# Kernel optimization log

Measured on AMD Instinct MI355X. Metric: run time of the kernel, lower is better.

Reference implementation:

```python
import jax, jax.numpy as jnp
import numpy as np

B, L, H = 32, 512, 1024
H2 = H // 2          # split half = 512
D_ATTN = 64
EPS = 1e-5


def setup_inputs() -> dict:
    key = jax.random.key(0)
    ks = jax.random.split(key, 6)
    x = jax.random.normal(ks[0], (B, L, H), dtype=jnp.float32)
    # LayerNorm params (default torch init: weight=1, bias=0)
    ln_gamma = jnp.ones((H2,), jnp.float32)
    ln_beta = jnp.zeros((H2,), jnp.float32)
    # Toeplitz params (module inits w_vector=0, bias=1; use small random w for nontrivial math)
    w_vector = jax.random.normal(ks[1], (2 * L - 1,), jnp.float32) * 0.02
    t_bias = jnp.ones((L,), jnp.float32)
    # TinyAttention: kqv Linear(H2 -> 3*d_attn), proj Linear(d_attn -> H2)
    kqv_w = jax.random.normal(ks[2], (H2, 3 * D_ATTN), jnp.float32) * 0.02
    kqv_b = jnp.zeros((3 * D_ATTN,), jnp.float32)
    proj_w = jax.random.normal(ks[3], (D_ATTN, H2), jnp.float32) * 0.02
    proj_b = jnp.zeros((H2,), jnp.float32)
    return {"x": x, "ln_gamma": ln_gamma, "ln_beta": ln_beta,
            "w_vector": w_vector, "t_bias": t_bias,
            "kqv_w": kqv_w, "kqv_b": kqv_b, "proj_w": proj_w, "proj_b": proj_b}


def _toeplitz(w_vector):
    # Faithful replication of get_toeplitz(): pad, tile, trim, reshape, crop.
    r = w_vector.shape[0] // 2            # = L - 1
    t = jnp.pad(w_vector, (0, L))         # length 3L - 1
    t = jnp.tile(t, L)[:-L]               # length L * (3L - 2)
    t = t.reshape(L, 3 * L - 2)
    return t[:, r:-r]                      # [L, L]


def _tiny_attention(v, kqv_w, kqv_b, proj_w, proj_b):
    kqv = v @ kqv_w + kqv_b                        # [B, L, 3*d_attn]
    k, q, val = jnp.split(kqv, 3, axis=-1)         # chunk order: key, query, value
    scale = 1.0 / jnp.sqrt(jnp.float32(q.shape[-1]))
    scores = jnp.einsum('bqd,bkd->bqk', q, k) * scale
    soft = jax.nn.softmax(scores, axis=-1)
    head = jnp.einsum('bqk,bkd->bqd', soft, val)   # [B, L, d_attn]
    return head @ proj_w + proj_b                  # [B, L, H2]


def reference(x, ln_gamma, ln_beta, w_vector, t_bias, kqv_w, kqv_b, proj_w, proj_b):
    u, v = jnp.split(x, 2, axis=-1)                # each [B, L, H2]
    head = _tiny_attention(v, kqv_w, kqv_b, proj_w, proj_b)
    # LayerNorm over last dim
    mu = jnp.mean(v, axis=-1, keepdims=True)
    var = jnp.mean(jnp.square(v - mu), axis=-1, keepdims=True)
    vn = (v - mu) * jax.lax.rsqrt(var + EPS) * ln_gamma + ln_beta
    # spatial (Toeplitz) mixing: permute -> [B, H2, L], matmul [L, L], bias
    w_t = _toeplitz(w_vector)
    vm = jnp.einsum('blc,lm->bmc', vn, w_t.T).transpose(0, 2, 1)  # keep faithful: vp @ w_t
    vm = jnp.einsum('bcl,lm->bcm', vn.transpose(0, 2, 1), w_t) + t_bias
    v_out = vm.transpose(0, 2, 1) + head           # [B, L, H2]
    return u * v_out
```

## Files before the change

### kernel.cpp

```cpp
#include <hip/hip_runtime.h>
#include <math.h>

#define NB 32
#define LL 512
#define HH 1024
#define H2 512
#define DA 64

typedef unsigned int u32;
typedef unsigned short u16;
typedef __bf16 bf16x8 __attribute__((ext_vector_type(8)));
typedef float f32x4 __attribute__((ext_vector_type(4)));

__device__ __forceinline__ u16 f2bu(float f) {
    u32 u = __builtin_bit_cast(u32, f);
    u = (u + 0x7fff + ((u >> 16) & 1)) >> 16;
    return (u16)u;
}

__device__ __forceinline__ float b2f(u16 u) {
    u32 v = (u32)u << 16;
    return __builtin_bit_cast(float, v);
}

__device__ __forceinline__ void async_cp16(const void* g, void* l) {
    __builtin_amdgcn_global_load_lds(
        (const __attribute__((address_space(1))) u32*)g,
        (__attribute__((address_space(3))) u32*)l, 16, 0, 0);
}

__global__ void prep_kernel(const float* __restrict__ wv,
                            const float* __restrict__ kqvw,
                            const float* __restrict__ projw,
                            u16* __restrict__ wt, u16* __restrict__ kqvwT,
                            u16* __restrict__ projwT) {
    int e = blockIdx.x * 256 + threadIdx.x;
    if (e < 262144) {
        int m = e >> 9, l = e & 511;
        wt[e] = f2bu(wv[511 + m - l]);
    } else if (e < 262144 + 98304) {
        int i = e - 262144;
        int n = i >> 9, k = i & 511;
        kqvwT[i] = f2bu(kqvw[(size_t)k * 192 + n]);
    } else {
        int i = e - 360448;
        int c = i >> 6, d = i & 63;
        projwT[i] = f2bu(projw[(size_t)d * 512 + c]);
    }
}

__global__ __launch_bounds__(512, 4)
void front_kernel(const float* __restrict__ x,
                  const float* __restrict__ gamma, const float* __restrict__ beta,
                  u16* __restrict__ vnT) {
    __shared__ u16 T[512 * 36];
    int blk = blockIdx.x, t = threadIdx.x;
    int b = blk >> 4, l0 = (blk & 15) * 32;
    int r = t >> 4, cl = t & 15;
    int rs = r ^ ((cl & 3) << 3);
    const float* xr = x + ((size_t)(b * LL + l0 + r)) * HH + H2;

    float4 v[8];
#pragma unroll
    for (int i = 0; i < 8; ++i) v[i] = *(const float4*)(xr + i * 64 + cl * 4);
    float s1 = 0.0f, s2 = 0.0f;
#pragma unroll
    for (int i = 0; i < 8; ++i) {
        s1 += v[i].x + v[i].y + v[i].z + v[i].w;
        s2 += v[i].x * v[i].x + v[i].y * v[i].y + v[i].z * v[i].z + v[i].w * v[i].w;
    }
    s1 += __shfl_xor(s1, 1); s2 += __shfl_xor(s2, 1);
    s1 += __shfl_xor(s1, 2); s2 += __shfl_xor(s2, 2);
    s1 += __shfl_xor(s1, 4); s2 += __shfl_xor(s2, 4);
    s1 += __shfl_xor(s1, 8); s2 += __shfl_xor(s2, 8);
    float mu = s1 * (1.0f / H2);
    float rstd = rsqrtf(s2 * (1.0f / H2) - mu * mu + 1e-5f);

#pragma unroll
    for (int hh = 0; hh < 2; ++hh) {
        float4 g[4], be[4];
#pragma unroll
        for (int i = 0; i < 4; ++i) {
            g[i]  = *(const float4*)(gamma + (hh * 4 + i) * 64 + cl * 4);
            be[i] = *(const float4*)(beta  + (hh * 4 + i) * 64 + cl * 4);
        }
#pragma unroll
        for (int i = 0; i < 4; ++i) {
            int ii = hh * 4 + i;
            int c = ii * 64 + cl * 4;
            float4 vv = v[ii];
            T[(c + 0) * 36 + rs] = f2bu((vv.x - mu) * rstd * g[i].x + be[i].x);
            T[(c + 1) * 36 + rs] = f2bu((vv.y - mu) * rstd * g[i].y + be[i].y);
            T[(c + 2) * 36 + rs] = f2bu((vv.z - mu) * rstd * g[i].z + be[i].z);
            T[(c + 3) * 36 + rs] = f2bu((vv.w - mu) * rstd * g[i].w + be[i].w);
        }
    }
    __syncthreads();

    int c = t;
    int swzB = ((c >> 2) & 3) << 3;
    const u16* Tp = T + c * 36;
    ushort4 o[8];
#pragma unroll
    for (int h = 0; h < 8; ++h)
        o[h] = *(const ushort4*)(Tp + ((h << 2) ^ swzB));
    u16* dst = vnT + ((size_t)(b * H2 + c)) * LL + l0;
#pragma unroll
    for (int h = 0; h < 4; ++h) {
        union { ushort4 u2[2]; uint4 q; } pk;
        pk.u2[0] = o[2 * h]; pk.u2[1] = o[2 * h + 1];
        ((uint4*)dst)[h] = pk.q;
    }
}

__global__ __launch_bounds__(256, 4)
void kqv_kernel(const float* __restrict__ x,
                const u16* __restrict__ kqvwT, const float* __restrict__ kqvb,
                u16* __restrict__ qb, u16* __restrict__ kb, u16* __restrict__ vT) {
    __shared__ u16 Ks[16 * 64];
    __shared__ u16 Qs[16 * 64];
    __shared__ u16 Vs[64 * 40];
    int blk = blockIdx.x, t = threadIdx.x;
    int R0 = blk * 16;
    int b = R0 >> 9, l0 = R0 & 511;
    int lane = t & 63, wid = t >> 6;
    int l15 = lane & 15, q16 = lane >> 4, q8 = q16 * 8;
    int n0 = wid * 48;
    const float* xa = x + ((size_t)(R0 + l15)) * HH + H2;
    const u16* Bb = kqvwT + (size_t)(n0 + l15) * 512;

    f32x4 acc[3] = {};
    float4 a0 = *(const float4*)(xa + q8);
    float4 a1 = *(const float4*)(xa + q8 + 4);
    bf16x8 b0 = *(const bf16x8*)(Bb + 0 * 8192 + q8);
    bf16x8 b1 = *(const bf16x8*)(Bb + 1 * 8192 + q8);
    bf16x8 b2 = *(const bf16x8*)(Bb + 2 * 8192 + q8);
#pragma unroll
    for (int it = 0; it < 16; ++it) {
        float4 na0, na1; bf16x8 nb0, nb1, nb2;
        if (it < 15) {
            int ko = (it + 1) * 32 + q8;
            na0 = *(const float4*)(xa + ko);
            na1 = *(const float4*)(xa + ko + 4);
            nb0 = *(const bf16x8*)(Bb + 0 * 8192 + ko);
            nb1 = *(const bf16x8*)(Bb + 1 * 8192 + ko);
            nb2 = *(const bf16x8*)(Bb + 2 * 8192 + ko);
        }
        bf16x8 a;
        a[0] = __builtin_bit_cast(__bf16, f2bu(a0.x));
        a[1] = __builtin_bit_cast(__bf16, f2bu(a0.y));
        a[2] = __builtin_bit_cast(__bf16, f2bu(a0.z));
        a[3] = __builtin_bit_cast(__bf16, f2bu(a0.w));
        a[4] = __builtin_bit_cast(__bf16, f2bu(a1.x));
        a[5] = __builtin_bit_cast(__bf16, f2bu(a1.y));
        a[6] = __builtin_bit_cast(__bf16, f2bu(a1.z));
        a[7] = __builtin_bit_cast(__bf16, f2bu(a1.w));
        acc[0] = __builtin_amdgcn_mfma_f32_16x16x32_bf16(a, b0, acc[0], 0, 0, 0);
        acc[1] = __builtin_amdgcn_mfma_f32_16x16x32_bf16(a, b1, acc[1], 0, 0, 0);
        acc[2] = __builtin_amdgcn_mfma_f32_16x16x32_bf16(a, b2, acc[2], 0, 0, 0);
        a0 = na0; a1 = na1; b0 = nb0; b1 = nb1; b2 = nb2;
    }

    int rq = q16 * 4;
#pragma unroll
    for (int j = 0; j < 3; ++j) {
        int n = n0 + j * 16 + l15;
        float bias = kqvb[n];
#pragma unroll
        for (int rr = 0; rr < 4; ++rr) {
            int m = rq + rr;
            u16 hv = f2bu(acc[j][rr] + bias);
            if (n < 64)       Ks[m * 64 + n] = hv;
            else if (n < 128) Qs[m * 64 + (n - 64)] = hv;
            else              Vs[(n - 128) * 40 + m] = hv;
        }
    }
    __syncthreads();
    {
        size_t base = (size_t)R0 * 64;
        *(ushort4*)(kb + base + t * 4) = *(const ushort4*)(Ks + t * 4);
        *(ushort4*)(qb + base + t * 4) = *(const ushort4*)(Qs + t * 4);
        int d = t >> 2, ls = (t & 3) * 4;
        *(ushort4*)(vT + ((size_t)(b * 64 + d)) * 512 + l0 + ls) =
            *(const ushort4*)(Vs + d * 40 + ls);
    }
}

#define VLD 136
__global__ __launch_bounds__(256, 4)
void attn_kernel(const u16* __restrict__ qb, const u16* __restrict__ kb,
                 const u16* __restrict__ vT, u16* __restrict__ head) {
    __shared__ u16 Ps[4 * 16 * VLD];
    __shared__ float Osh[4][16 * 65];
    __shared__ float Msh[4][16], Lsh[4][16];
    int b = blockIdx.y, q0 = blockIdx.x * 16;
    int t = threadIdx.x, lane = t & 63, w = t >> 6;
    int l15 = lane & 15, q16 = lane >> 4, q8 = q16 * 8;
    int kc = w * 128;
    const u16* qg = qb + (size_t)b * LL * DA;
    const u16* kg = kb + (size_t)b * LL * DA;
    const u16* vg = vT + (size_t)b * DA * LL;

    bf16x8 aq[2];
#pragma unroll
    for (int s = 0; s < 2; ++s)
        aq[s] = *(const bf16x8*)(qg + (size_t)(q0 + l15) * DA + s * 32 + q8);

    f32x4 sc[8] = {};
#pragma unroll
    for (int j = 0; j < 8; ++j) {
#pragma unroll
        for (int s = 0; s < 2; ++s) {
            bf16x8 bk = *(const bf16x8*)(kg + (size_t)(kc + j * 16 + l15) * DA + s * 32 + q8);
            sc[j] = __builtin_amdgcn_mfma_f32_16x16x32_bf16(aq[s], bk, sc[j], 0, 0, 0);
        }
    }
    float mx[4], sm[4];
#pragma unroll
    for (int j = 0; j < 8; ++j)
#pragma unroll
        for (int rr = 0; rr < 4; ++rr) sc[j][rr] *= 0.125f;
#pragma unroll
    for (int rr = 0; rr < 4; ++rr) {
        float m0 = sc[0][rr];
#pragma unroll
        for (int j = 1; j < 8; ++j) m0 = fmaxf(m0, sc[j][rr]);
        m0 = fmaxf(m0, __shfl_xor(m0, 1));
        m0 = fmaxf(m0, __shfl_xor(m0, 2));
        m0 = fmaxf(m0, __shfl_xor(m0, 4));
        m0 = fmaxf(m0, __shfl_xor(m0, 8));
        mx[rr] = m0;
    }
#pragma unroll
    for (int j = 0; j < 8; ++j)
#pragma unroll
        for (int rr = 0; rr < 4; ++rr) sc[j][rr] = __expf(sc[j][rr] - mx[rr]);
#pragma unroll
    for (int rr = 0; rr < 4; ++rr) {
        float s0 = sc[0][rr];
#pragma unroll
        for (int j = 1; j < 8; ++j) s0 += sc[j][rr];
        s0 += __shfl_xor(s0, 1);
        s0 += __shfl_xor(s0, 2);
        s0 += __shfl_xor(s0, 4);
        s0 += __shfl_xor(s0, 8);
        sm[rr] = s0;
    }
    u16* Pw = Ps + w * 16 * VLD;
#pragma unroll
    for (int j = 0; j < 8; ++j)
#pragma unroll
        for (int rr = 0; rr < 4; ++rr)
            Pw[(q16 * 4 + rr) * VLD + j * 16 + l15] = f2bu(sc[j][rr]);
    f32x4 o[4] = {};
#pragma unroll
    for (int kt = 0; kt < 4; ++kt) {
        bf16x8 ap = *(const bf16x8*)(Pw + l15 * VLD + kt * 32 + q8);
#pragma unroll
        for (int j = 0; j < 4; ++j) {
            bf16x8 bv = *(const bf16x8*)(vg + (size_t)(j * 16 + l15) * LL + kc + kt * 32 + q8);
            o[j] = __builtin_amdgcn_mfma_f32_16x16x32_bf16(ap, bv, o[j], 0, 0, 0);
        }
    }
#pragma unroll
    for (int j = 0; j < 4; ++j)
#pragma unroll
        for (int rr = 0; rr < 4; ++rr)
            Osh[w][(q16 * 4 + rr) * 65 + j * 16 + l15] = o[j][rr];
    if (l15 == 0) {
#pragma unroll
        for (int rr = 0; rr < 4; ++rr) {
            Msh[w][q16 * 4 + rr] = mx[rr];
            Lsh[w][q16 * 4 + rr] = sm[rr];
        }
    }
    __syncthreads();
    int qq = t >> 4, dg = (t & 15) * 4;
    float m0 = Msh[0][qq], m1 = Msh[1][qq], m2 = Msh[2][qq], m3 = Msh[3][qq];
    float ms = fmaxf(fmaxf(m0, m1), fmaxf(m2, m3));
    float f0 = __expf(m0 - ms), f1 = __expf(m1 - ms), f2 = __expf(m2 - ms), f3 = __expf(m3 - ms);
    float lst = Lsh[0][qq] * f0 + Lsh[1][qq] * f1 + Lsh[2][qq] * f2 + Lsh[3][qq] * f3;
    float inv = 1.0f / lst;
    ushort4 res;
    u16* rp = (u16*)&res;
#pragma unroll
    for (int i = 0; i < 4; ++i) {
        int idx = qq * 65 + dg + i;
        float a = Osh[0][idx] * f0 + Osh[1][idx] * f1 + Osh[2][idx] * f2 + Osh[3][idx] * f3;
        rp[i] = f2bu(a * inv);
    }
    *(ushort4*)(head + (size_t)(b * LL + q0 + qq) * DA + dg) = res;
}

__device__ __forceinline__ void mfma_tile64(const u16* As, const u16* Bs,
                                            f32x4 acc[4][4], int wm, int wn,
                                            int l15, int q16) {
    int s7 = l15 & 7;
#pragma unroll
    for (int kk = 0; kk < 2; ++kk) {
        int j0 = kk * 4 + q16;
        bf16x8 a[4], bv[4];
#pragma unroll
        for (int i = 0; i < 4; ++i) {
            int row = wm + i * 16 + l15;
            a[i] = *(const bf16x8*)(As + (row * 8 + (j0 ^ s7)) * 8);
        }
#pragma unroll
        for (int j = 0; j < 4; ++j) {
            int row = wn + j * 16 + l15;
            bv[j] = *(const bf16x8*)(Bs + (row * 8 + (j0 ^ s7)) * 8);
        }
#pragma unroll
        for (int i = 0; i < 4; ++i)
#pragma unroll
            for (int j = 0; j < 4; ++j)
                acc[i][j] = __builtin_amdgcn_mfma_f32_16x16x32_bf16(a[i], bv[j], acc[i][j], 0, 0, 0);
    }
}

__device__ __forceinline__ void stage_pair(const u16* A, const u16* B, int ldk,
                                           int koff, u16* Ad, u16* Bd, int t) {
#pragma unroll
    for (int s = 0; s < 4; ++s) {
        int ci = t + s * 256;
        int grow = ci >> 3, gcol = ((ci & 7) ^ (grow & 7)) << 3;
        async_cp16(A + (size_t)grow * ldk + koff + gcol, Ad + ci * 8);
        async_cp16(B + (size_t)grow * ldk + koff + gcol, Bd + ci * 8);
    }
}

__global__ __launch_bounds__(256, 2)
void mix_kernel(const u16* __restrict__ wt,
                const u16* __restrict__ vnT,
                const u16* __restrict__ headb,
                const u16* __restrict__ projwT,
                const float* __restrict__ x,
                const float* __restrict__ tbias,
                const float* __restrict__ projb,
                float* __restrict__ out) {
    __shared__ u16 As[2][128 * 64];
    __shared__ u16 Bs[2][128 * 64];
    int lid = blockIdx.x;
    int p8 = lid & 7, rest = lid >> 3;
    int mi = rest & 3, pair = (rest >> 2) * 8 + p8;
    int b = pair >> 2, m0 = mi * 128, c0 = (pair & 3) * 128;
    int t = threadIdx.x, lane = t & 63, wid = t >> 6;
    int wm = (wid >> 1) * 64, wn = (wid & 1) * 64;
    int l15 = lane & 15, q16 = lane >> 4;
    f32x4 acc[4][4] = {};
    const u16* Ag = wt + (size_t)m0 * 512;
    const u16* Bg = vnT + ((size_t)b * H2 + c0) * 512;
    const u16* Hg = headb + ((size_t)b * LL + m0) * DA;
    const u16* Pg = projwT + (size_t)c0 * DA;

    stage_pair(Ag, Bg, 512, 0, As[0], Bs[0], t);
    __syncthreads();

    for (int it = 0; it < 9; ++it) {
        int nx = it + 1;
        if (nx < 8)
            stage_pair(Ag, Bg, 512, nx * 64, As[nx & 1], Bs[nx & 1], t);
        else if (nx == 8)
            stage_pair(Hg, Pg, 64, 0, As[0], Bs[0], t);
        mfma_tile64(As[it & 1], Bs[it & 1], acc, wm, wn, l15, q16);
        __syncthreads();
    }

    int rq = q16 * 4;
#pragma unroll
    for (int i = 0; i < 4; ++i) {
#pragma unroll
        for (int rr = 0; rr < 4; ++rr) {
            int m = m0 + wm + i * 16 + rq + rr;
            float tb = tbias[m];
            const float* xrow = x + ((size_t)b * LL + m) * HH;
            float* orow = out + ((size_t)b * LL + m) * H2;
#pragma unroll
            for (int j = 0; j < 4; ++j) {
                int c = c0 + wn + j * 16 + l15;
                float val = acc[i][j][rr] + tb + projb[c];
                orow[c] = xrow[c] * val;
            }
        }
    }
}

extern "C" void kernel_launch(void* const* d_in, const int* in_sizes, int n_in,
                              void* d_out, int out_size, void* d_ws, size_t ws_size,
                              hipStream_t stream) {
    (void)in_sizes; (void)n_in; (void)out_size; (void)ws_size;
    const float* x     = (const float*)d_in[0];
    const float* gamma = (const float*)d_in[1];
    const float* beta  = (const float*)d_in[2];
    const float* wv    = (const float*)d_in[3];
    const float* tb    = (const float*)d_in[4];
    const float* kqvw  = (const float*)d_in[5];
    const float* kqvb  = (const float*)d_in[6];
    const float* projw = (const float*)d_in[7];
    const float* projb = (const float*)d_in[8];
    float* out = (float*)d_out;

    u16* vnT_bf  = (u16*)d_ws;
    u16* qb      = vnT_bf + (size_t)NB * LL * H2;
    u16* kb      = qb + (size_t)NB * LL * DA;
    u16* vTb     = kb + (size_t)NB * LL * DA;
    u16* head_bf = vTb + (size_t)NB * LL * DA;
    u16* wt_bf   = head_bf + (size_t)NB * LL * DA;
    u16* kqvwT   = wt_bf + 512 * 512;
    u16* projwT  = kqvwT + 192 * 512;

    prep_kernel <<<1536, 256, 0, stream>>>(wv, kqvw, projw, wt_bf, kqvwT, projwT);
    front_kernel<<<512, 512, 0, stream>>>(x, gamma, beta, vnT_bf);
    kqv_kernel  <<<1024, 256, 0, stream>>>(x, kqvwT, kqvb, qb, kb, vTb);
    attn_kernel <<<dim3(32, NB), 256, 0, stream>>>(qb, kb, vTb, head_bf);
    mix_kernel  <<<512, 256, 0, stream>>>(wt_bf, vnT_bf, head_bf, projwT,
                                          x, tb, projb, out);
}
```

Baseline: 201.7 us.

## Retile KQV projection to 64-row blocks with double-buffered LDS staging

The KQV projection kernel now gives each block 64 rows instead of 16, so each block loads the 192x512 weight matrix once per 64 rows rather than once per 16. Weight tiles go through LDS with async 16-byte copies and an XOR swizzle. Activation tiles are converted to bf16 and written to a padded LDS buffer, double-buffered so the next chunk loads while the current one runs on MFMA. The trade-off is a launch of 256 blocks instead of 1024, each using about 67 KB of LDS, so fewer blocks fit per CU and some CUs may sit idle; the output stores are also widened to 16 bytes.

```diff
diff --git a/kernel.cpp b/kernel.cpp
--- a/kernel.cpp
+++ b/kernel.cpp
@@ -113,76 +113,123 @@
     }
 }
 
-__global__ __launch_bounds__(256, 4)
+__global__ __launch_bounds__(256, 2)
 void kqv_kernel(const float* __restrict__ x,
                 const u16* __restrict__ kqvwT, const float* __restrict__ kqvb,
                 u16* __restrict__ qb, u16* __restrict__ kb, u16* __restrict__ vT) {
-    __shared__ u16 Ks[16 * 64];
-    __shared__ u16 Qs[16 * 64];
-    __shared__ u16 Vs[64 * 40];
+    __shared__ u16 As_[2][64 * 72];
+    __shared__ u16 Bs_[2][192 * 64];
     int blk = blockIdx.x, t = threadIdx.x;
-    int R0 = blk * 16;
+    int R0 = blk * 64;
     int b = R0 >> 9, l0 = R0 & 511;
     int lane = t & 63, wid = t >> 6;
     int l15 = lane & 15, q16 = lane >> 4, q8 = q16 * 8;
-    int n0 = wid * 48;
-    const float* xa = x + ((size_t)(R0 + l15)) * HH + H2;
-    const u16* Bb = kqvwT + (size_t)(n0 + l15) * 512;
-
-    f32x4 acc[3] = {};
-    float4 a0 = *(const float4*)(xa + q8);
-    float4 a1 = *(const float4*)(xa + q8 + 4);
-    bf16x8 b0 = *(const bf16x8*)(Bb + 0 * 8192 + q8);
-    bf16x8 b1 = *(const bf16x8*)(Bb + 1 * 8192 + q8);
-    bf16x8 b2 = *(const bf16x8*)(Bb + 2 * 8192 + q8);
-#pragma unroll
-    for (int it = 0; it < 16; ++it) {
-        float4 na0, na1; bf16x8 nb0, nb1, nb2;
-        if (it < 15) {
-            int ko = (it + 1) * 32 + q8;
-            na0 = *(const float4*)(xa + ko);
-            na1 = *(const float4*)(xa + ko + 4);
-            nb0 = *(const bf16x8*)(Bb + 0 * 8192 + ko);
-            nb1 = *(const bf16x8*)(Bb + 1 * 8192 + ko);
-            nb2 = *(const bf16x8*)(Bb + 2 * 8192 + ko);
-        }
-        bf16x8 a;
-        a[0] = __builtin_bit_cast(__bf16, f2bu(a0.x));
-        a[1] = __builtin_bit_cast(__bf16, f2bu(a0.y));
-        a[2] = __builtin_bit_cast(__bf16, f2bu(a0.z));
-        a[3] = __builtin_bit_cast(__bf16, f2bu(a0.w));
-        a[4] = __builtin_bit_cast(__bf16, f2bu(a1.x));
-        a[5] = __builtin_bit_cast(__bf16, f2bu(a1.y));
-        a[6] = __builtin_bit_cast(__bf16, f2bu(a1.z));
-        a[7] = __builtin_bit_cast(__bf16, f2bu(a1.w));
-        acc[0] = __builtin_amdgcn_mfma_f32_16x16x32_bf16(a, b0, acc[0], 0, 0, 0);
-        acc[1] = __builtin_amdgcn_mfma_f32_16x16x32_bf16(a, b1, acc[1], 0, 0, 0);
-        acc[2] = __builtin_amdgcn_mfma_f32_16x16x32_bf16(a, b2, acc[2], 0, 0, 0);
-        a0 = na0; a1 = na1; b0 = nb0; b1 = nb1; b2 = nb2;
-    }
-
+    int wm = (wid & 1) * 32, wn = (wid >> 1) * 96;
+    const float* xg = x + (size_t)R0 * HH + H2;
+
+    int arow[4], af4[4];
+#pragma unroll
+    for (int p = 0; p < 4; ++p) {
+        int flat = t + p * 256;
+        arow[p] = flat >> 4; af4[p] = flat & 15;
+    }
+
+    f32x4 acc[2][6] = {};
+    float4 av[4];
+
+#pragma unroll
+    for (int p = 0; p < 4; ++p)
+        av[p] = *(const float4*)(xg + (size_t)arow[p] * HH + af4[p] * 4);
+#pragma unroll
+    for (int s = 0; s < 6; ++s) {
+        int ci = t + s * 256;
+        int grow = ci >> 3, gcol = ((ci & 7) ^ (grow & 7)) << 3;
+        async_cp16(kqvwT + (size_t)grow * 512 + gcol, &Bs_[0][ci * 8]);
+    }
+#pragma unroll
+    for (int p = 0; p < 4; ++p) {
+        ushort4 pk;
+        pk.x = f2bu(av[p].x); pk.y = f2bu(av[p].y);
+        pk.z = f2bu(av[p].z); pk.w = f2bu(av[p].w);
+        *(ushort4*)(&As_[0][arow[p] * 72 + af4[p] * 4]) = pk;
+    }
+    __syncthreads();
+
+    for (int it = 0; it < 8; ++it) {
+        int nx = it + 1, nb = nx & 1, cb = it & 1;
+        if (it < 7) {
+            int k0n = nx * 64;
+#pragma unroll
+            for (int p = 0; p < 4; ++p)
+                av[p] = *(const float4*)(xg + (size_t)arow[p] * HH + k0n + af4[p] * 4);
+#pragma unroll
+            for (int s = 0; s < 6; ++s) {
+                int ci = t + s * 256;
+                int grow = ci >> 3, gcol = ((ci & 7) ^ (grow & 7)) << 3;
+                async_cp16(kqvwT + (size_t)grow * 512 + k0n + gcol, &Bs_[nb][ci * 8]);
+            }
+        }
+        const u16* Ap = &As_[cb][0];
+        const u16* Bp = &Bs_[cb][0];
+#pragma unroll
+        for (int kk = 0; kk < 2; ++kk) {
+            int j0 = kk * 4 + q16;
+            bf16x8 a[2];
+#pragma unroll
+            for (int i = 0; i < 2; ++i)
+                a[i] = *(const bf16x8*)(Ap + (wm + i * 16 + l15) * 72 + kk * 32 + q8);
+#pragma unroll
+            for (int j = 0; j < 6; ++j) {
+                int n = wn + j * 16 + l15;
+                bf16x8 bb = *(const bf16x8*)(Bp + (n * 8 + (j0 ^ (n & 7))) * 8);
+#pragma unroll
+                for (int i = 0; i < 2; ++i)
+                    acc[i][j] = __builtin_amdgcn_mfma_f32_16x16x32_bf16(a[i], bb, acc[i][j], 0, 0, 0);
+            }
+        }
+        if (it < 7) {
+#pragma unroll
+            for (int p = 0; p < 4; ++p) {
+                ushort4 pk;
+                pk.x = f2bu(av[p].x); pk.y = f2bu(av[p].y);
+                pk.z = f2bu(av[p].z); pk.w = f2bu(av[p].w);
+                *(ushort4*)(&As_[nb][arow[p] * 72 + af4[p] * 4]) = pk;
+            }
+        }
+        __syncthreads();
+    }
+
+    u16* Ks = &As_[0][0];
+    u16* Qs = &As_[1][0];
+    u16* Vs = &Bs_[0][0];
     int rq = q16 * 4;
 #pragma unroll
-    for (int j = 0; j < 3; ++j) {
-        int n = n0 + j * 16 + l15;
-        float bias = kqvb[n];
-#pragma unroll
-        for (int rr = 0; rr < 4; ++rr) {
-            int m = rq + rr;
-            u16 hv = f2bu(acc[j][rr] + bias);
-            if (n < 64)       Ks[m * 64 + n] = hv;
-            else if (n < 128) Qs[m * 64 + (n - 64)] = hv;
-            else              Vs[(n - 128) * 40 + m] = hv;
+    for (int i = 0; i < 2; ++i) {
+#pragma unroll
+        for (int j = 0; j < 6; ++j) {
+            int n = wn + j * 16 + l15;
+            float bias = kqvb[n];
+#pragma unroll
+            for (int rr = 0; rr < 4; ++rr) {
+                int m = wm + i * 16 + rq + rr;
+                u16 hv = f2bu(acc[i][j][rr] + bias);
+                if (n < 64)       Ks[m * 64 + n] = hv;
+                else if (n < 128) Qs[m * 64 + (n - 64)] = hv;
+                else              Vs[(n - 128) * 72 + m] = hv;
+            }
         }
     }
     __syncthreads();
     {
-        size_t base = (size_t)R0 * 64;
-        *(ushort4*)(kb + base + t * 4) = *(const ushort4*)(Ks + t * 4);
-        *(ushort4*)(qb + base + t * 4) = *(const ushort4*)(Qs + t * 4);
-        int d = t >> 2, ls = (t & 3) * 4;
-        *(ushort4*)(vT + ((size_t)(b * 64 + d)) * 512 + l0 + ls) =
-            *(const ushort4*)(Vs + d * 40 + ls);
+        size_t base = (size_t)R0 * 64 + t * 16;
+        *(uint4*)(kb + base)     = *(const uint4*)(Ks + t * 16);
+        *(uint4*)(kb + base + 8) = *(const uint4*)(Ks + t * 16 + 8);
+        *(uint4*)(qb + base)     = *(const uint4*)(Qs + t * 16);
+        *(uint4*)(qb + base + 8) = *(const uint4*)(Qs + t * 16 + 8);
+        int d = t >> 2, ls = (t & 3) * 16;
+        u16* vd = vT + ((size_t)(b * 64 + d)) * 512 + l0 + ls;
+        *(uint4*)(vd)     = *(const uint4*)(Vs + d * 72 + ls);
+        *(uint4*)(vd + 8) = *(const uint4*)(Vs + d * 72 + ls + 8);
     }
 }
 
@@ -411,7 +458,7 @@
 
     prep_kernel <<<1536, 256, 0, stream>>>(wv, kqvw, projw, wt_bf, kqvwT, projwT);
     front_kernel<<<512, 512, 0, stream>>>(x, gamma, beta, vnT_bf);
-    kqv_kernel  <<<1024, 256, 0, stream>>>(x, kqvwT, kqvb, qb, kb, vTb);
+    kqv_kernel  <<<256, 256, 0, stream>>>(x, kqvwT, kqvb, qb, kb, vTb);
     attn_kernel <<<dim3(32, NB), 256, 0, stream>>>(qb, kb, vTb, head_bf);
     mix_kernel  <<<512, 256, 0, stream>>>(wt_bf, vnT_bf, head_bf, projwT,
                                           x, tb, projb, out);
```

Result: faster. 181.4 us (-10.1%).
